# Optimization experiments

Hardware: AMD Instinct MI355X
Metric: run time of the kernel (lower is better)

## Reference

```python
import jax, jax.numpy as jnp
import numpy as np

WS = 8      # window size (all three entries equal)
NH = 4      # num_heads
CE = 32     # exp_channels = layer_size[0]


def _sine_pos(h, w, npf, temperature=10000.0):
    # faithful port of get_sine_position_encoding(HW=(h,w), num_pos_feats=npf, normalize=True)
    scale = 2.0 * np.pi
    eps = 1e-6
    y = np.cumsum(np.ones((1, h, w), np.float32), 1)
    xg = np.cumsum(np.ones((1, h, w), np.float32), 2)
    y = y / (y[:, -1:, :] + eps) * scale
    xg = xg / (xg[:, :, -1:] + eps) * scale
    dim_t = temperature ** (2.0 * (np.arange(npf) // 2) / npf)
    px = xg[..., None] / dim_t
    py = y[..., None] / dim_t
    px = np.stack((np.sin(px[..., 0::2]), np.cos(px[..., 1::2])), -1).reshape(1, h, w, npf)
    py = np.stack((np.sin(py[..., 0::2]), np.cos(py[..., 1::2])), -1).reshape(1, h, w, npf)
    return jnp.asarray(np.concatenate((py, px), -1).reshape(1, h * w, 2 * npf), jnp.float32)


def _rel_pos_index(a, b):
    coords = np.stack(np.meshgrid(np.arange(a), np.arange(b), indexing='ij')).reshape(2, -1)
    rel = (coords[:, :, None] - coords[:, None, :]).transpose(1, 2, 0).copy()
    rel[..., 0] += a - 1
    rel[..., 1] += b - 1
    rel[..., 0] *= 2 * b - 1
    return jnp.asarray(rel.sum(-1).astype(np.int32))


POS_BIAS = _sine_pos(WS, WS, CE // 2)   # (1, 64, 32)
RPI = _rel_pos_index(WS, WS)            # (64, 64) int


def _ln(x, g, b, eps=1e-5):
    mu = x.mean(-1, keepdims=True)
    var = jnp.mean((x - mu) ** 2, -1, keepdims=True)
    return (x - mu) / jnp.sqrt(var + eps) * g + b


def _geglu(x, w11, b11, w12, b12, w2, b2):
    return (jax.nn.gelu(x @ w11.T + b11, approximate=False) * (x @ w12.T + b12)) @ w2.T + b2


def _forward(x, ln1_g, ln1_b, w_ea, w_sa, rpb_table, fc11_w, fc11_b, fc12_w, fc12_b, fc2_w, fc2_b, ln2_g, ln2_b, m11_w, m11_b, m12_w, m12_b, m2_w, m2_b):
    B, E, C, H, W = x.shape
    h, w = H // WS, W // WS
    N = WS * WS
    nW = h * w
    scale = C ** (-0.5)
    x_origin = x
    # window partition (matches torch view/permute/contiguous-view exactly)
    xw = x.reshape(B, E, C, h, WS, w, WS).transpose(0, 1, 3, 5, 2, 4, 6).reshape(-1, N, C)
    xw = _ln(xw, ln1_g, ln1_b)
    # fused QKV projections
    qkv_ea = ((xw + POS_BIAS) @ w_ea.T).reshape(B, 4, nW, N, 3, NH, C)
    qkv_ea = qkv_ea.transpose(1, 4, 0, 2, 5, 3, 6).reshape(4, 3, B * nW, NH, N, C)   # E nP (B nW) nH W C
    qkv_sa = (xw @ w_sa.T).reshape(B, 4, nW, N, 3, NH, C)
    qkv_sa = qkv_sa.transpose(4, 0, 2, 5, 3, 1, 6).reshape(3, B * nW, NH, N, 4 * C)  # nP (B nW) nH W (E C)

    def attn(q, k, v, bias=None):
        s = jnp.einsum('bhid,bhjd->bhij', q * scale, k)
        if bias is not None:
            s = s + bias
        return jnp.einsum('bhij,bhjd->bhid', jax.nn.softmax(s, axis=-1), v)

    # exposure-alignment branches (the Python loop over 4 exposures, vectorized)
    ea1 = jax.vmap(attn, in_axes=(None, 0, 0))(qkv_ea[0, 0], qkv_ea[:, 1], qkv_ea[:, 2])
    ea2 = jax.vmap(attn, in_axes=(0, None, None))(qkv_ea[:, 0], qkv_ea[0, 1], qkv_ea[0, 2])

    def merge(o):  # (4, BnW, NH, N, C) -> cat over exposures on channels -> (BnW, N, NH*4C)
        o = jnp.moveaxis(o, 0, 3).reshape(B * nW, NH, N, 4 * C)
        return o.transpose(0, 2, 1, 3).reshape(B * nW, N, NH * 4 * C)

    ea1, ea2 = merge(ea1), merge(ea2)
    # self-attention branch with relative position bias gather
    bias = rpb_table[RPI.reshape(-1)].reshape(N, N, NH).transpose(2, 0, 1)[None]
    sa = attn(qkv_sa[0], qkv_sa[1], qkv_sa[2], bias)
    sa = sa.transpose(0, 2, 1, 3).reshape(B * nW, N, NH * 4 * C)

    y = jnp.concatenate([sa, ea1, ea2], axis=-1)                      # (BnW, N, 12*NH*C)
    y = _geglu(y, fc11_w, fc11_b, fc12_w, fc12_b, fc2_w, fc2_b)       # (BnW, N, 4C)
    # window reverse (matches torch view/permute/view exactly)
    y = y.reshape(B, h, w, WS, WS, 4, NH, C // NH).transpose(0, 5, 6, 7, 3, 1, 4, 2).reshape(B, 4, C, H, W)
    x1 = y + x_origin
    t = x1.transpose(0, 3, 4, 1, 2).reshape(B, H, W, 4 * C)           # B N C H W -> B H W (N C)
    t = _ln(t, ln2_g, ln2_b)
    t = _geglu(t, m11_w, m11_b, m12_w, m12_b, m2_w, m2_b)
    t = t.reshape(B, H, W, 4, C).transpose(0, 3, 4, 1, 2)
    return x1 + t


def setup_inputs() -> dict:
    key = jax.random.key(0)
    ks = jax.random.split(key, 10)
    f32 = jnp.float32
    return {
        'x': jax.random.normal(ks[0], (2, 4, 32, 128, 128), f32),
        'ln1_g': jnp.ones((32,), f32),
        'ln1_b': jnp.zeros((32,), f32),
        'w_ea': 0.02 * jax.random.normal(ks[1], (384, 32), f32),
        'w_sa': 0.02 * jax.random.normal(ks[2], (384, 32), f32),
        'rpb_table': 0.02 * jax.random.normal(ks[3], (225, 4), f32),
        'fc11_w': 0.02 * jax.random.normal(ks[4], (128, 1536), f32),
        'fc11_b': jnp.zeros((128,), f32),
        'fc12_w': 0.02 * jax.random.normal(ks[5], (128, 1536), f32),
        'fc12_b': jnp.zeros((128,), f32),
        'fc2_w': 0.02 * jax.random.normal(ks[6], (128, 128), f32),
        'fc2_b': jnp.zeros((128,), f32),
        'ln2_g': jnp.ones((128,), f32),
        'ln2_b': jnp.zeros((128,), f32),
        'm11_w': 0.02 * jax.random.normal(ks[7], (128, 128), f32),
        'm11_b': jnp.zeros((128,), f32),
        'm12_w': 0.02 * jax.random.normal(ks[8], (128, 128), f32),
        'm12_b': jnp.zeros((128,), f32),
        'm2_w': 0.02 * jax.random.normal(ks[9], (128, 128), f32),
        'm2_b': jnp.zeros((128,), f32),
    }


def reference(x, ln1_g, ln1_b, w_ea, w_sa, rpb_table, fc11_w, fc11_b, fc12_w, fc12_b, fc2_w, fc2_b, ln2_g, ln2_b, m11_w, m11_b, m12_w, m12_b, m2_w, m2_b):
    return _forward(x, ln1_g, ln1_b, w_ea, w_sa, rpb_table, fc11_w, fc11_b, fc12_w, fc12_b, fc2_w, fc2_b, ln2_g, ln2_b, m11_w, m11_b, m12_w, m12_b, m2_w, m2_b)
```

## Files before the change

kernel.cpp:

```cpp
#include <hip/hip_runtime.h>
#include <hip/hip_bf16.h>
#include <cstdint>

#define SCALE 0.17677669529663687f

typedef float f4v __attribute__((ext_vector_type(4)));
typedef short s4v __attribute__((ext_vector_type(4)));
typedef short short8 __attribute__((ext_vector_type(8)));

__device__ __forceinline__ float b2f(short s){
  return __uint_as_float(((unsigned)(unsigned short)s) << 16);
}
__device__ __forceinline__ short f2b(float f){
  unsigned u = __float_as_uint(f);
  unsigned r = (u + 0x7fffu + ((u >> 16) & 1u)) >> 16;
  return (short)r;
}
__device__ __forceinline__ float geluf(float x){
  return 0.5f * x * (1.0f + erff(x * 0.7071067811865476f));
}
__device__ __forceinline__ f4v MFMA(short8 a, short8 b, f4v c){
  return __builtin_amdgcn_mfma_f32_16x16x32_bf16(a, b, c, 0, 0, 0);
}
__device__ __forceinline__ short8 ldsA(const short* base, int ld, int rowBase, int kBase, int l){
  return *(const short8*)(base + (rowBase + (l & 15)) * ld + kBase + ((l >> 4) << 3));
}
__device__ __forceinline__ short8 pack8(f4v a0, f4v a1, float scl){
  short8 o;
  #pragma unroll
  for (int k = 0; k < 4; ++k){
    o[k]     = f2b(a0[k] * scl);
    o[k + 4] = f2b(a1[k] * scl);
  }
  return o;
}
__device__ __forceinline__ int permTok(int n){
  return (n & 32) | (((n >> 2) & 3) << 3) | (((n >> 4) & 1) << 2) | (n & 3);
}

#define MTP_S   0
#define FWP1_S  8192
#define FWP2_S  204800
#define FC2_S   401408
#define M11_S   417792
#define M12_S   434176
#define M2_S    450560
#define POS_S   466944
#define BIASP_B 937984
#define YW_B    1048576

__global__ void prep(const float* __restrict__ wea, const float* __restrict__ wsa,
                     const float* __restrict__ fc11, const float* __restrict__ fc12,
                     const float* __restrict__ fc2,  const float* __restrict__ m11,
                     const float* __restrict__ m12,  const float* __restrict__ m2,
                     const float* __restrict__ rpb,
                     short* __restrict__ wsS, float* __restrict__ biasP)
{
  int gid = blockIdx.x * 256 + threadIdx.x;
  int stride = gridDim.x * 256;
  for (int id = gid; id < 786432; id += stride){
    int isB = (id >= 393216);
    int i2 = isB ? id - 393216 : id;
    const float* fc = isB ? fc12 : fc11;
    int blk = i2 >> 12, rem = i2 & 4095;
    int o = rem >> 5, s = rem & 31;
    int h4 = (s >> 3) & 3, kp = s & 7;
    int c = 16*(kp >> 2) + 4*h4 + (kp & 3);
    int br = blk >> 4, h = (blk >> 2) & 3, e = blk & 3;
    int cb = h*128 + e*32 + (br == 0 ? 0 : (br == 1 ? 512 : 1024));
    const float* w = (br == 0) ? wsa : wea;
    float acc = 0.f;
    for (int f = 0; f < 32; ++f)
      acc += fc[o*1536 + cb + f] * w[(256 + h*32 + f)*32 + c];
    wsS[(isB ? FWP2_S : FWP1_S) + blk*4096 + o*32 + s] = f2b(acc);
  }
  for (int id = gid; id < 8192; id += stride){
    int u = id >> 10, jp = (id >> 5) & 31, a = id & 31;
    int h = u & 3;
    const float* w = (u < 4) ? wsa : wea;
    int t = jp >> 4, h4 = (jp >> 2) & 3, r = jp & 3;
    int b = 8*h4 + 4*t + r;
    float acc = 0.f;
    for (int d = 0; d < 32; ++d)
      acc += w[(h*32 + d)*32 + a] * w[(128 + h*32 + d)*32 + b];
    wsS[MTP_S + u*1024 + jp*32 + a] = f2b(acc * SCALE);
  }
  for (int id = gid; id < 65536; id += stride){
    const float* src; int base; int off = id & 16383;
    switch (id >> 14){
      case 0:  src = fc2; base = FC2_S; break;
      case 1:  src = m11; base = M11_S; break;
      case 2:  src = m12; base = M12_S; break;
      default: src = m2;  base = M2_S;  break;
    }
    wsS[base + off] = f2b(src[off]);
  }
  for (int id = gid; id < 16384; id += stride){
    int hh = id >> 12, i = (id >> 6) & 63, h4 = (id >> 4) & 3, tj = (id >> 2) & 3, r = id & 3;
    int j = tj*16 + 4*h4 + r;
    int idx = ((i >> 3) - (j >> 3) + 7)*15 + ((i & 7) - (j & 7) + 7);
    biasP[id] = rpb[idx*4 + hh];
  }
  if (gid < 64){
    const float invT[8] = {1.f, 0.316227766f, 0.1f, 0.0316227766f,
                           0.01f, 0.00316227766f, 0.001f, 0.000316227766f};
    const float ANG = 6.28318530717958647692f / 8.000001f;
    float ay = (float)((gid >> 3) + 1) * ANG;
    float ax = (float)((gid & 7) + 1) * ANG;
    #pragma unroll
    for (int m = 0; m < 8; ++m){
      float s, cc;
      sincosf(ay * invT[m], &s, &cc);
      wsS[POS_S + gid*32 + 2*m]      = f2b(s);
      wsS[POS_S + gid*32 + 2*m + 1]  = f2b(cc);
      sincosf(ax * invT[m], &s, &cc);
      wsS[POS_S + gid*32 + 16 + 2*m] = f2b(s);
      wsS[POS_S + gid*32 + 17 + 2*m] = f2b(cc);
    }
  }
}

struct __align__(16) SmemA {
  short xw_ab[8704];
  short xtp_gb[16896];
};

__device__ __forceinline__ float smax16(f4v* s){
  float m = s[0][0];
  #pragma unroll
  for (int tj = 0; tj < 4; ++tj)
    #pragma unroll
    for (int r = 0; r < 4; ++r) m = fmaxf(m, s[tj][r]);
  m = fmaxf(m, __shfl_xor(m, 16));
  m = fmaxf(m, __shfl_xor(m, 32));
  float sum = 0.f;
  #pragma unroll
  for (int tj = 0; tj < 4; ++tj)
    #pragma unroll
    for (int r = 0; r < 4; ++r){
      float e = expf(s[tj][r] - m);
      s[tj][r] = e;
      sum += e;
    }
  sum += __shfl_xor(sum, 16);
  sum += __shfl_xor(sum, 32);
  return 1.0f / sum;
}

__device__ __forceinline__ short8 projXq(const short* mtp, const short* xwE,
                                         int rho, int l){
  short8 xa = *(const short8*)(xwE + (rho*16 + (l & 15))*32 + ((l >> 4) << 3));
  f4v q0 = {0.f,0.f,0.f,0.f}, q1 = {0.f,0.f,0.f,0.f};
  q0 = MFMA(*(const short8*)(mtp + (l & 15)*32 + ((l >> 4) << 3)), xa, q0);
  q1 = MFMA(*(const short8*)(mtp + (16 + (l & 15))*32 + ((l >> 4) << 3)), xa, q1);
  return pack8(q0, q1, 1.f);
}

__device__ __forceinline__ void geglu16(short8 rp, const short* wsS, int blk,
                                        f4v* g1, f4v* g2, int l){
  const short* f1 = wsS + FWP1_S + blk*4096 + (l & 15)*32 + ((l >> 4) << 3);
  #pragma unroll
  for (int ct = 0; ct < 8; ++ct)
    g1[ct] = MFMA(rp, *(const short8*)(f1 + ct*512), g1[ct]);
  const short* f2 = wsS + FWP2_S + blk*4096 + (l & 15)*32 + ((l >> 4) << 3);
  #pragma unroll
  for (int ct = 0; ct < 8; ++ct)
    g2[ct] = MFMA(rp, *(const short8*)(f2 + ct*512), g2[ct]);
}

__device__ __forceinline__ void unitTail(f4v* s, const short* xtpE, const short* wsS,
                                         int blk, int blkFold, f4v* g1, f4v* g2, int l){
  float inv = smax16(s);
  short8 pk0 = pack8(s[0], s[1], 1.f);
  short8 pk1 = pack8(s[2], s[3], 1.f);
  f4v rt0 = {0.f,0.f,0.f,0.f}, rt1 = {0.f,0.f,0.f,0.f};
  const short* x0 = xtpE + (l & 15)*72 + ((l >> 4) << 3);
  const short* x1 = xtpE + (16 + (l & 15))*72 + ((l >> 4) << 3);
  rt0 = MFMA(*(const short8*)(x0), pk0, rt0);
  rt0 = MFMA(*(const short8*)(x0 + 32), pk1, rt0);
  rt1 = MFMA(*(const short8*)(x1), pk0, rt1);
  rt1 = MFMA(*(const short8*)(x1 + 32), pk1, rt1);
  short8 rp = pack8(rt0, rt1, inv);
  geglu16(rp, wsS, blk, g1, g2, l);
  if (blkFold >= 0) geglu16(rp, wsS, blkFold, g1, g2, l);
}

__global__ __launch_bounds__(512, 4) void kernelA(
    const float* __restrict__ x,
    const float* __restrict__ ln1g, const float* __restrict__ ln1b,
    const float* __restrict__ fc11b_, const float* __restrict__ fc12b_,
    const float* __restrict__ fc2b_,
    const short* __restrict__ wsS, const float* __restrict__ biasP,
    short* __restrict__ yw)
{
  __shared__ SmemA sm;
  short* xw  = sm.xw_ab;
  short* ab  = sm.xw_ab;
  short* xtp = sm.xtp_gb;
  float* gb  = (float*)sm.xtp_gb;

  const int t = threadIdx.x, l = t & 63, w = t >> 6;
  const int tau = w >> 2, rho = w & 3;
  const int bw = blockIdx.x, b = bw >> 8, hw = bw & 255, hi = hw >> 4, wj = hw & 15;
  const int row0 = rho*16 + ((l >> 4) << 2);
  const short* posb = wsS + POS_S;

  {
    const int e = w & 3, n = l;
    const int c = n >> 1, i0 = (n & 1) * 4;
    const float* src = x + ((size_t)((b*4 + e)*32 + c) * 128 + hi*8) * 128 + wj*8;
    float v[32];
    #pragma unroll
    for (int ii = 0; ii < 4; ++ii){
      f4v a  = *(const f4v*)(src + (size_t)(i0 + ii)*128);
      f4v bb = *(const f4v*)(src + (size_t)(i0 + ii)*128 + 4);
      v[ii*8+0]=a[0]; v[ii*8+1]=a[1]; v[ii*8+2]=a[2]; v[ii*8+3]=a[3];
      v[ii*8+4]=bb[0]; v[ii*8+5]=bb[1]; v[ii*8+6]=bb[2]; v[ii*8+7]=bb[3];
    }
    float mu = 0.f;
    #pragma unroll
    for (int k = 0; k < 32; ++k) mu += v[k];
    mu *= (1.f/32.f);
    float var = 0.f;
    #pragma unroll
    for (int k = 0; k < 32; ++k){ float d = v[k]-mu; var += d*d; }
    var *= (1.f/32.f);
    float rstd = rsqrtf(var + 1e-5f);
    if (w < 4){
      #pragma unroll
      for (int c4 = 0; c4 < 8; ++c4){
        s4v sv;
        #pragma unroll
        for (int j = 0; j < 4; ++j)
          sv[j] = f2b((v[c4*4+j]-mu)*rstd*ln1g[c4*4+j] + ln1b[c4*4+j]);
        *(s4v*)&xw[e*2048 + n*32 + c4*4] = sv;
      }
    } else {
      int pn = permTok(n);
      #pragma unroll
      for (int c2 = 0; c2 < 32; ++c2)
        xtp[e*2304 + c2*72 + pn] = f2b((v[c2]-mu)*rstd*ln1g[c2] + ln1b[c2]);
    }
  }
  __syncthreads();

  f4v g1[8], g2[8];
  #pragma unroll
  for (int i = 0; i < 8; ++i){
    g1[i] = (f4v){0.f,0.f,0.f,0.f};
    g2[i] = (f4v){0.f,0.f,0.f,0.f};
  }

  #pragma unroll 1
  for (int hx = 0; hx < 2; ++hx){
    const int hh = tau*2 + hx;
    const short* mtp = wsS + MTP_S + hh*1024;
    f4v s[4];
    #pragma unroll
    for (int i = 0; i < 4; ++i) s[i] = (f4v){0.f,0.f,0.f,0.f};
    #pragma unroll
    for (int e = 0; e < 4; ++e){
      short8 xq = projXq(mtp, xw + e*2048, rho, l);
      #pragma unroll
      for (int tj = 0; tj < 4; ++tj)
        s[tj] = MFMA(ldsA(xw + e*2048, 32, tj*16, 0, l), xq, s[tj]);
    }
    const float* bb = biasP + ((hh*64 + rho*16 + (l & 15))*4 + (l >> 4)) * 16;
    #pragma unroll
    for (int tj = 0; tj < 4; ++tj){
      f4v bv = *(const f4v*)(bb + tj*4);
      s[tj] += bv;
    }
    float inv = smax16(s);
    short8 pk0 = pack8(s[0], s[1], 1.f);
    short8 pk1 = pack8(s[2], s[3], 1.f);
    #pragma unroll 1
    for (int dc = 0; dc < 4; ++dc){
      const short* xt = xtp + dc*2304;
      f4v rt0 = {0.f,0.f,0.f,0.f}, rt1 = {0.f,0.f,0.f,0.f};
      const short* x0 = xt + (l & 15)*72 + ((l >> 4) << 3);
      const short* x1 = xt + (16 + (l & 15))*72 + ((l >> 4) << 3);
      rt0 = MFMA(*(const short8*)(x0), pk0, rt0);
      rt0 = MFMA(*(const short8*)(x0 + 32), pk1, rt0);
      rt1 = MFMA(*(const short8*)(x1), pk0, rt1);
      rt1 = MFMA(*(const short8*)(x1 + 32), pk1, rt1);
      short8 rp = pack8(rt0, rt1, inv);
      geglu16(rp, wsS, hh*4 + dc, g1, g2, l);
    }
  }

  __syncthreads();
  {
    const int e = w & 3, n = l;
    if (w < 4){
      #pragma unroll
      for (int c4 = 0; c4 < 8; ++c4){
        s4v xa = *(const s4v*)&xw[e*2048 + n*32 + c4*4];
        s4v pa = *(const s4v*)(posb + n*32 + c4*4);
        s4v o;
        #pragma unroll
        for (int j = 0; j < 4; ++j) o[j] = f2b(b2f(xa[j]) + b2f(pa[j]));
        *(s4v*)&xw[e*2048 + n*32 + c4*4] = o;
      }
    } else {
      int pn = permTok(n);
      #pragma unroll
      for (int c2 = 0; c2 < 32; ++c2){
        int idx = e*2304 + c2*72 + pn;
        xtp[idx] = f2b(b2f(xtp[idx]) + b2f(posb[n*32 + c2]));
      }
    }
  }
  __syncthreads();

  #pragma unroll 1
  for (int hx = 0; hx < 2; ++hx){
    const int hh = tau*2 + hx;
    const short* mtp = wsS + MTP_S + (4 + hh)*1024;
    #pragma unroll 1
    for (int e = 0; e < 4; ++e){
      short8 xq = projXq(mtp, xw + e*2048, rho, l);
      f4v s[4];
      #pragma unroll
      for (int i = 0; i < 4; ++i) s[i] = (f4v){0.f,0.f,0.f,0.f};
      #pragma unroll
      for (int tj = 0; tj < 4; ++tj)
        s[tj] = MFMA(ldsA(xw, 32, tj*16, 0, l), xq, s[tj]);
      unitTail(s, xtp, wsS, 32 + hh*4 + e, (e == 0) ? (16 + hh*4) : -1, g1, g2, l);
    }
    short8 xq0 = projXq(mtp, xw, rho, l);
    #pragma unroll 1
    for (int e = 1; e < 4; ++e){
      f4v s[4];
      #pragma unroll
      for (int i = 0; i < 4; ++i) s[i] = (f4v){0.f,0.f,0.f,0.f};
      #pragma unroll
      for (int tj = 0; tj < 4; ++tj)
        s[tj] = MFMA(ldsA(xw + e*2048, 32, tj*16, 0, l), xq0, s[tj]);
      unitTail(s, xtp + e*2304, wsS, 16 + hh*4 + e, -1, g1, g2, l);
    }
  }

  __syncthreads();
  if (tau == 1){
    #pragma unroll
    for (int ct = 0; ct < 8; ++ct)
      #pragma unroll
      for (int r = 0; r < 4; ++r)
        gb[(row0 + r)*132 + ct*16 + (l & 15)] = g1[ct][r];
  }
  __syncthreads();
  if (tau == 0){
    #pragma unroll
    for (int ct = 0; ct < 8; ++ct)
      #pragma unroll
      for (int r = 0; r < 4; ++r)
        g1[ct][r] += gb[(row0 + r)*132 + ct*16 + (l & 15)];
  }
  __syncthreads();
  if (tau == 1){
    #pragma unroll
    for (int ct = 0; ct < 8; ++ct)
      #pragma unroll
      for (int r = 0; r < 4; ++r)
        gb[(row0 + r)*132 + ct*16 + (l & 15)] = g2[ct][r];
  }
  __syncthreads();
  if (tau == 0){
    #pragma unroll
    for (int ct = 0; ct < 8; ++ct){
      int o = ct*16 + (l & 15);
      float b1 = fc11b_[o], b2 = fc12b_[o];
      #pragma unroll
      for (int r = 0; r < 4; ++r){
        float h2 = g2[ct][r] + gb[(row0 + r)*132 + o] + b2;
        ab[(row0 + r)*136 + o] = f2b(geluf(g1[ct][r] + b1) * h2);
      }
    }
  }
  __syncthreads();
  {
    const short* fc2 = wsS + FC2_S;
    f4v z[4];
    #pragma unroll
    for (int i = 0; i < 4; ++i) z[i] = (f4v){0.f,0.f,0.f,0.f};
    #pragma unroll
    for (int ks = 0; ks < 4; ++ks){
      short8 a = ldsA(ab, 136, rho*16, ks*32, l);
      #pragma unroll
      for (int ctl = 0; ctl < 4; ++ctl){
        int ct2 = tau*4 + ctl;
        short8 bfrag = *(const short8*)(fc2 + (ct2*16 + (l & 15))*128 + ks*32 + ((l >> 4) << 3));
        z[ctl] = MFMA(a, bfrag, z[ctl]);
      }
    }
    short* ywb = yw + (size_t)bw * 8192;
    #pragma unroll
    for (int ctl = 0; ctl < 4; ++ctl){
      int o = (tau*4 + ctl)*16 + (l & 15);
      float bz = fc2b_[o];
      #pragma unroll
      for (int r = 0; r < 4; ++r)
        ywb[(row0 + r)*128 + o] = f2b(z[ctl][r] + bz);
    }
  }
}

struct SmemB {
  float x1t[128][132];
  short xnt[128][136];
  short ab[64][136];
};

__global__ __launch_bounds__(256) void kernelB(
    const float* __restrict__ x,
    const float* __restrict__ ln2g, const float* __restrict__ ln2b,
    const float* __restrict__ m11b, const float* __restrict__ m12b,
    const float* __restrict__ m2b,
    const short* __restrict__ wsS, const short* __restrict__ yw,
    float* __restrict__ out)
{
  __shared__ SmemB sm;
  const int t = threadIdx.x, l = t & 63, w = t >> 6;
  const int b = blockIdx.x >> 7, rr = blockIdx.x & 127;
  const short* m11 = wsS + M11_S;
  const short* m12 = wsS + M12_S;
  const short* m2  = wsS + M2_S;
  const float* xb = x + (size_t)b * 128 * 16384 + (size_t)rr * 128;

  for (int fid = t; fid < 4096; fid += 256){
    int ch = fid >> 5, q4 = fid & 31;
    *(f4v*)&sm.x1t[ch][q4*4] = *(const f4v*)(xb + (size_t)ch * 16384 + q4*4);
  }
  __syncthreads();
  {
    int q = t >> 1, hf = t & 1;
    const short* ys = yw + ((size_t)(b*256 + (rr & 15)*16 + (q & 15)) * 64
                            + (rr >> 4)*8 + (q >> 4)) * 128 + hf*64;
    #pragma unroll
    for (int k = 0; k < 64; ++k)
      sm.x1t[hf*64 + k][q] += b2f(ys[k]);
  }
  __syncthreads();
  {
    int q = t >> 1, hf = t & 1;
    float s = 0.f;
    for (int i = 0; i < 64; ++i) s += sm.x1t[hf*64 + i][q];
    s += __shfl_xor(s, 1);
    float mu = s * (1.f/128.f);
    float vv = 0.f;
    for (int i = 0; i < 64; ++i){ float d = sm.x1t[hf*64 + i][q] - mu; vv += d*d; }
    vv += __shfl_xor(vv, 1);
    float rstd = rsqrtf(vv * (1.f/128.f) + 1e-5f);
    for (int i4 = 0; i4 < 16; ++i4){
      s4v o;
      #pragma unroll
      for (int j = 0; j < 4; ++j){
        int ch = hf*64 + i4*4 + j;
        o[j] = f2b((sm.x1t[ch][q] - mu) * rstd * ln2g[ch] + ln2b[ch]);
      }
      *(s4v*)&sm.xnt[q][hf*64 + i4*4] = o;
    }
  }
  __syncthreads();
  for (int qb = 0; qb < 2; ++qb){
    int px0 = qb*64 + w*16;
    f4v G1[8], G2[8];
    #pragma unroll
    for (int i = 0; i < 8; ++i){
      G1[i] = (f4v){0.f,0.f,0.f,0.f};
      G2[i] = (f4v){0.f,0.f,0.f,0.f};
    }
    #pragma unroll
    for (int ks = 0; ks < 4; ++ks){
      short8 a = ldsA(&sm.xnt[0][0], 136, px0, ks*32, l);
      const short* p1 = m11 + (l & 15)*128 + ks*32 + ((l >> 4) << 3);
      #pragma unroll
      for (int ct = 0; ct < 8; ++ct)
        G1[ct] = MFMA(a, *(const short8*)(p1 + ct*16*128), G1[ct]);
      const short* p2 = m12 + (l & 15)*128 + ks*32 + ((l >> 4) << 3);
      #pragma unroll
      for (int ct = 0; ct < 8; ++ct)
        G2[ct] = MFMA(a, *(const short8*)(p2 + ct*16*128), G2[ct]);
    }
    int r0 = w*16 + ((l >> 4) << 2);
    #pragma unroll
    for (int ct = 0; ct < 8; ++ct){
      int o = ct*16 + (l & 15);
      float bb1 = m11b[o], bb2 = m12b[o];
      #pragma unroll
      for (int r = 0; r < 4; ++r)
        sm.ab[r0 + r][o] = f2b(geluf(G1[ct][r] + bb1) * (G2[ct][r] + bb2));
    }
    __syncthreads();
    f4v Z[8];
    #pragma unroll
    for (int i = 0; i < 8; ++i) Z[i] = (f4v){0.f,0.f,0.f,0.f};
    #pragma unroll
    for (int ks = 0; ks < 4; ++ks){
      short8 a = ldsA(&sm.ab[0][0], 136, w*16, ks*32, l);
      const short* pz = m2 + (l & 15)*128 + ks*32 + ((l >> 4) << 3);
      #pragma unroll
      for (int ct = 0; ct < 8; ++ct)
        Z[ct] = MFMA(a, *(const short8*)(pz + ct*16*128), Z[ct]);
    }
    #pragma unroll
    for (int ct = 0; ct < 8; ++ct){
      int ch = ct*16 + (l & 15);
      float bz = m2b[ch];
      #pragma unroll
      for (int r = 0; r < 4; ++r){
        int px = px0 + ((l >> 4) << 2) + r;
        sm.x1t[ch][px] += Z[ct][r] + bz;
      }
    }
    __syncthreads();
  }
  {
    int ch = t >> 1, qh = t & 1;
    float* ob = out + ((size_t)b*128 + ch) * 16384 + (size_t)rr * 128 + qh*64;
    #pragma unroll
    for (int q4 = 0; q4 < 16; ++q4)
      *(f4v*)(ob + q4*4) = *(const f4v*)&sm.x1t[ch][qh*64 + q4*4];
  }
}

extern "C" void kernel_launch(void* const* d_in, const int* in_sizes, int n_in,
                              void* d_out, int out_size, void* d_ws, size_t ws_size,
                              hipStream_t stream) {
  (void)in_sizes; (void)n_in; (void)out_size; (void)ws_size;
  const float* x     = (const float*)d_in[0];
  const float* ln1g  = (const float*)d_in[1];
  const float* ln1b  = (const float*)d_in[2];
  const float* wea   = (const float*)d_in[3];
  const float* wsa   = (const float*)d_in[4];
  const float* rpb   = (const float*)d_in[5];
  const float* fc11w = (const float*)d_in[6];
  const float* fc11b = (const float*)d_in[7];
  const float* fc12w = (const float*)d_in[8];
  const float* fc12b = (const float*)d_in[9];
  const float* fc2w  = (const float*)d_in[10];
  const float* fc2b  = (const float*)d_in[11];
  const float* ln2g  = (const float*)d_in[12];
  const float* ln2b  = (const float*)d_in[13];
  const float* m11w  = (const float*)d_in[14];
  const float* m11b  = (const float*)d_in[15];
  const float* m12w  = (const float*)d_in[16];
  const float* m12b  = (const float*)d_in[17];
  const float* m2w   = (const float*)d_in[18];
  const float* m2b   = (const float*)d_in[19];

  short* wsS   = (short*)d_ws;
  float* biasP = (float*)((char*)d_ws + BIASP_B);
  short* yw    = (short*)((char*)d_ws + YW_B);

  prep<<<1024, 256, 0, stream>>>(wea, wsa, fc11w, fc12w, fc2w, m11w, m12w, m2w,
                                 rpb, wsS, biasP);
  kernelA<<<512, 512, 0, stream>>>(x, ln1g, ln1b, fc11b, fc12b, fc2b,
                                   wsS, biasP, yw);
  kernelB<<<256, 256, 0, stream>>>(x, ln2g, ln2b, m11b, m12b, m2b,
                                   wsS, yw, (float*)d_out);
}
```

Baseline: 245.4 us.

## Halve kernelA block to 256 threads, each wave handling all heads

```diff
diff --git a/kernel.cpp b/kernel.cpp
--- a/kernel.cpp
+++ b/kernel.cpp
@@ -122,7 +122,7 @@
 
 struct __align__(16) SmemA {
   short xw_ab[8704];
-  short xtp_gb[16896];
+  short xtp[9216];
 };
 
 __device__ __forceinline__ float smax16(f4v* s){
@@ -185,7 +185,7 @@
   if (blkFold >= 0) geglu16(rp, wsS, blkFold, g1, g2, l);
 }
 
-__global__ __launch_bounds__(512, 4) void kernelA(
+__global__ __launch_bounds__(256, 3) void kernelA(
     const float* __restrict__ x,
     const float* __restrict__ ln1g, const float* __restrict__ ln1b,
     const float* __restrict__ fc11b_, const float* __restrict__ fc12b_,
@@ -196,17 +196,16 @@
   __shared__ SmemA sm;
   short* xw  = sm.xw_ab;
   short* ab  = sm.xw_ab;
-  short* xtp = sm.xtp_gb;
-  float* gb  = (float*)sm.xtp_gb;
+  short* xtp = sm.xtp;
 
   const int t = threadIdx.x, l = t & 63, w = t >> 6;
-  const int tau = w >> 2, rho = w & 3;
+  const int rho = w;
   const int bw = blockIdx.x, b = bw >> 8, hw = bw & 255, hi = hw >> 4, wj = hw & 15;
   const int row0 = rho*16 + ((l >> 4) << 2);
   const short* posb = wsS + POS_S;
 
   {
-    const int e = w & 3, n = l;
+    const int e = w, n = l;
     const int c = n >> 1, i0 = (n & 1) * 4;
     const float* src = x + ((size_t)((b*4 + e)*32 + c) * 128 + hi*8) * 128 + wj*8;
     float v[32];
@@ -226,21 +225,17 @@
     for (int k = 0; k < 32; ++k){ float d = v[k]-mu; var += d*d; }
     var *= (1.f/32.f);
     float rstd = rsqrtf(var + 1e-5f);
-    if (w < 4){
-      #pragma unroll
-      for (int c4 = 0; c4 < 8; ++c4){
-        s4v sv;
-        #pragma unroll
-        for (int j = 0; j < 4; ++j)
-          sv[j] = f2b((v[c4*4+j]-mu)*rstd*ln1g[c4*4+j] + ln1b[c4*4+j]);
-        *(s4v*)&xw[e*2048 + n*32 + c4*4] = sv;
-      }
-    } else {
-      int pn = permTok(n);
-      #pragma unroll
-      for (int c2 = 0; c2 < 32; ++c2)
-        xtp[e*2304 + c2*72 + pn] = f2b((v[c2]-mu)*rstd*ln1g[c2] + ln1b[c2]);
-    }
+    short lnv[32];
+    #pragma unroll
+    for (int c2 = 0; c2 < 32; ++c2)
+      lnv[c2] = f2b((v[c2]-mu)*rstd*ln1g[c2] + ln1b[c2]);
+    #pragma unroll
+    for (int c4 = 0; c4 < 8; ++c4)
+      *(s4v*)&xw[e*2048 + n*32 + c4*4] = *(const s4v*)&lnv[c4*4];
+    int pn = permTok(n);
+    #pragma unroll
+    for (int c2 = 0; c2 < 32; ++c2)
+      xtp[e*2304 + c2*72 + pn] = lnv[c2];
   }
   __syncthreads();
 
@@ -252,8 +247,7 @@
   }
 
   #pragma unroll 1
-  for (int hx = 0; hx < 2; ++hx){
-    const int hh = tau*2 + hx;
+  for (int hh = 0; hh < 4; ++hh){
     const short* mtp = wsS + MTP_S + hh*1024;
     f4v s[4];
     #pragma unroll
@@ -291,31 +285,27 @@
 
   __syncthreads();
   {
-    const int e = w & 3, n = l;
-    if (w < 4){
-      #pragma unroll
-      for (int c4 = 0; c4 < 8; ++c4){
-        s4v xa = *(const s4v*)&xw[e*2048 + n*32 + c4*4];
-        s4v pa = *(const s4v*)(posb + n*32 + c4*4);
-        s4v o;
-        #pragma unroll
-        for (int j = 0; j < 4; ++j) o[j] = f2b(b2f(xa[j]) + b2f(pa[j]));
-        *(s4v*)&xw[e*2048 + n*32 + c4*4] = o;
-      }
-    } else {
-      int pn = permTok(n);
-      #pragma unroll
-      for (int c2 = 0; c2 < 32; ++c2){
-        int idx = e*2304 + c2*72 + pn;
-        xtp[idx] = f2b(b2f(xtp[idx]) + b2f(posb[n*32 + c2]));
-      }
+    const int e = w, n = l;
+    #pragma unroll
+    for (int c4 = 0; c4 < 8; ++c4){
+      s4v xa = *(const s4v*)&xw[e*2048 + n*32 + c4*4];
+      s4v pa = *(const s4v*)(posb + n*32 + c4*4);
+      s4v o;
+      #pragma unroll
+      for (int j = 0; j < 4; ++j) o[j] = f2b(b2f(xa[j]) + b2f(pa[j]));
+      *(s4v*)&xw[e*2048 + n*32 + c4*4] = o;
+    }
+    int pn = permTok(n);
+    #pragma unroll
+    for (int c2 = 0; c2 < 32; ++c2){
+      int idx = e*2304 + c2*72 + pn;
+      xtp[idx] = f2b(b2f(xtp[idx]) + b2f(posb[n*32 + c2]));
     }
   }
   __syncthreads();
 
   #pragma unroll 1
-  for (int hx = 0; hx < 2; ++hx){
-    const int hh = tau*2 + hx;
+  for (int hh = 0; hh < 4; ++hh){
     const short* mtp = wsS + MTP_S + (4 + hh)*1024;
     #pragma unroll 1
     for (int e = 0; e < 4; ++e){
@@ -342,66 +332,39 @@
   }
 
   __syncthreads();
-  if (tau == 1){
-    #pragma unroll
-    for (int ct = 0; ct < 8; ++ct)
-      #pragma unroll
-      for (int r = 0; r < 4; ++r)
-        gb[(row0 + r)*132 + ct*16 + (l & 15)] = g1[ct][r];
-  }
-  __syncthreads();
-  if (tau == 0){
-    #pragma unroll
-    for (int ct = 0; ct < 8; ++ct)
-      #pragma unroll
-      for (int r = 0; r < 4; ++r)
-        g1[ct][r] += gb[(row0 + r)*132 + ct*16 + (l & 15)];
-  }
-  __syncthreads();
-  if (tau == 1){
-    #pragma unroll
-    for (int ct = 0; ct < 8; ++ct)
-      #pragma unroll
-      for (int r = 0; r < 4; ++r)
-        gb[(row0 + r)*132 + ct*16 + (l & 15)] = g2[ct][r];
-  }
-  __syncthreads();
-  if (tau == 0){
+  {
     #pragma unroll
     for (int ct = 0; ct < 8; ++ct){
       int o = ct*16 + (l & 15);
       float b1 = fc11b_[o], b2 = fc12b_[o];
       #pragma unroll
-      for (int r = 0; r < 4; ++r){
-        float h2 = g2[ct][r] + gb[(row0 + r)*132 + o] + b2;
-        ab[(row0 + r)*136 + o] = f2b(geluf(g1[ct][r] + b1) * h2);
-      }
+      for (int r = 0; r < 4; ++r)
+        ab[(row0 + r)*136 + o] = f2b(geluf(g1[ct][r] + b1) * (g2[ct][r] + b2));
     }
   }
   __syncthreads();
   {
     const short* fc2 = wsS + FC2_S;
-    f4v z[4];
-    #pragma unroll
-    for (int i = 0; i < 4; ++i) z[i] = (f4v){0.f,0.f,0.f,0.f};
+    f4v z[8];
+    #pragma unroll
+    for (int i = 0; i < 8; ++i) z[i] = (f4v){0.f,0.f,0.f,0.f};
     #pragma unroll
     for (int ks = 0; ks < 4; ++ks){
       short8 a = ldsA(ab, 136, rho*16, ks*32, l);
       #pragma unroll
-      for (int ctl = 0; ctl < 4; ++ctl){
-        int ct2 = tau*4 + ctl;
-        short8 bfrag = *(const short8*)(fc2 + (ct2*16 + (l & 15))*128 + ks*32 + ((l >> 4) << 3));
-        z[ctl] = MFMA(a, bfrag, z[ctl]);
+      for (int ct = 0; ct < 8; ++ct){
+        short8 bfrag = *(const short8*)(fc2 + (ct*16 + (l & 15))*128 + ks*32 + ((l >> 4) << 3));
+        z[ct] = MFMA(a, bfrag, z[ct]);
       }
     }
     short* ywb = yw + (size_t)bw * 8192;
     #pragma unroll
-    for (int ctl = 0; ctl < 4; ++ctl){
-      int o = (tau*4 + ctl)*16 + (l & 15);
+    for (int ct = 0; ct < 8; ++ct){
+      int o = ct*16 + (l & 15);
       float bz = fc2b_[o];
       #pragma unroll
       for (int r = 0; r < 4; ++r)
-        ywb[(row0 + r)*128 + o] = f2b(z[ctl][r] + bz);
+        ywb[(row0 + r)*128 + o] = f2b(z[ct][r] + bz);
     }
   }
 }
@@ -556,7 +519,7 @@
 
   prep<<<1024, 256, 0, stream>>>(wea, wsa, fc11w, fc12w, fc2w, m11w, m12w, m2w,
                                  rpb, wsS, biasP);
-  kernelA<<<512, 512, 0, stream>>>(x, ln1g, ln1b, fc11b, fc12b, fc2b,
+  kernelA<<<512, 256, 0, stream>>>(x, ln1g, ln1b, fc11b, fc12b, fc2b,
                                    wsS, biasP, yw);
   kernelB<<<256, 256, 0, stream>>>(x, ln2g, ln2b, m11b, m12b, m2b,
                                    wsS, yw, (float*)d_out);
```

Result: slower. 302.9 us (+23.4%).
